# Optimization experiments

Measured on AMD Instinct MI355X. Metric: run time of the kernel, lower is better.

## Reference

```python
import jax, jax.numpy as jnp
import numpy as np

D_MODEL = 512
NUM_HEADS = 8
D_HEAD = D_MODEL // NUM_HEADS


def setup_inputs() -> dict:
    key = jax.random.key(0)
    ks = jax.random.split(key, 9)
    B, L = 4, 2048
    s = 1.0 / np.sqrt(D_MODEL)
    inp = {
        "x": jax.random.normal(ks[0], (B, L, D_MODEL), dtype=jnp.float32),
        "Wq": jax.random.uniform(ks[1], (D_MODEL, D_MODEL), jnp.float32, -s, s),
        "bq": jax.random.uniform(ks[2], (D_MODEL,), jnp.float32, -s, s),
        "Wk": jax.random.uniform(ks[3], (D_MODEL, D_MODEL), jnp.float32, -s, s),
        "bk": jax.random.uniform(ks[4], (D_MODEL,), jnp.float32, -s, s),
        "Wv": jax.random.uniform(ks[5], (D_MODEL, D_MODEL), jnp.float32, -s, s),
        "bv": jax.random.uniform(ks[6], (D_MODEL,), jnp.float32, -s, s),
        "Wo": jax.random.uniform(ks[7], (D_MODEL, D_MODEL), jnp.float32, -s, s),
        "bo": jax.random.uniform(ks[8], (D_MODEL,), jnp.float32, -s, s),
    }
    return inp


def reference(x, Wq, bq, Wk, bk, Wv, bv, Wo, bo):
    B, L, _ = x.shape
    def split_heads(t):  # [B,L,D] -> [B,H,L,d]
        return t.reshape(B, L, NUM_HEADS, D_HEAD).transpose(0, 2, 1, 3)
    Q = split_heads(x @ Wq + bq)
    K = split_heads(x @ Wk + bk)
    V = split_heads(x @ Wv + bv)
    scale = 1.0 / jnp.sqrt(jnp.asarray(D_HEAD, dtype=x.dtype))
    scores = jnp.einsum('bhqd,bhkd->bhqk', Q, K) * scale  # [B,H,L,L]
    weights = jax.nn.softmax(scores, axis=-1)
    z = jnp.einsum('bhqk,bhkd->bhqd', weights, V)  # [B,H,L,d]
    z = z.transpose(0, 2, 1, 3).reshape(B, L, D_MODEL)
    return z @ Wo + bo
```

## Files before the change

### kernel.cpp

```cpp
#include <hip/hip_runtime.h>
#include <hip/hip_bf16.h>
#include <math.h>


#define MDIM 8192
#define DMODEL 512
#define NHEAD 8
#define DHEAD 64
#define LSEQ 2048

typedef __attribute__((ext_vector_type(8))) short short8;
typedef __attribute__((ext_vector_type(4))) float floatx4;

struct alignas(16) bf16x8 { __hip_bfloat16 v[8]; };
struct alignas(8)  bf16x4 { __hip_bfloat16 v[4]; };

__device__ __forceinline__ void load_lds16(const __hip_bfloat16* g, __hip_bfloat16* l) {
    __builtin_amdgcn_global_load_lds(
        (const __attribute__((address_space(1))) void*)g,
        (__attribute__((address_space(3))) void*)l,
        16, 0, 0);
}

__device__ __forceinline__ float fast_exp2(float x) {
#if __has_builtin(__builtin_amdgcn_exp2f)
    return __builtin_amdgcn_exp2f(x);
#else
    return __expf(x * 0.69314718055994531f);
#endif
}

__global__ __launch_bounds__(256) void cast_x_kernel(
    const float* __restrict__ x, __hip_bfloat16* __restrict__ xb)
{
    size_t i = ((size_t)blockIdx.x * 256 + threadIdx.x) * 8;
    float4 a = *reinterpret_cast<const float4*>(x + i);
    float4 b = *reinterpret_cast<const float4*>(x + i + 4);
    bf16x8 o;
    o.v[0] = __float2bfloat16(a.x); o.v[1] = __float2bfloat16(a.y);
    o.v[2] = __float2bfloat16(a.z); o.v[3] = __float2bfloat16(a.w);
    o.v[4] = __float2bfloat16(b.x); o.v[5] = __float2bfloat16(b.y);
    o.v[6] = __float2bfloat16(b.z); o.v[7] = __float2bfloat16(b.w);
    *reinterpret_cast<bf16x8*>(xb + i) = o;
}

__global__ __launch_bounds__(256) void transpose_cast_w(
    const float* __restrict__ Wq, const float* __restrict__ Wk,
    const float* __restrict__ Wv, const float* __restrict__ Wo,
    __hip_bfloat16* __restrict__ Wt)
{
    __shared__ float t[32][33];
    const int z = blockIdx.z;
    const float* W = z == 0 ? Wq : (z == 1 ? Wk : (z == 2 ? Wv : Wo));
    __hip_bfloat16* dst = Wt + ((size_t)z << 18);
    int k0 = blockIdx.x * 32, n0 = blockIdx.y * 32;
    int c = threadIdx.x & 31, r = threadIdx.x >> 5;
    #pragma unroll
    for (int i = 0; i < 4; ++i)
        t[r + 8 * i][c] = W[(size_t)(k0 + r + 8 * i) * DMODEL + n0 + c];
    __syncthreads();
    #pragma unroll
    for (int i = 0; i < 4; ++i)
        dst[(size_t)(n0 + r + 8 * i) * DMODEL + k0 + c] = __float2bfloat16(t[c][r + 8 * i]);
}

__global__ __launch_bounds__(256) void gemm_qkv_mfma(
    const __hip_bfloat16* __restrict__ xb,
    const __hip_bfloat16* __restrict__ Wt,
    const float* __restrict__ bq, const float* __restrict__ bk,
    const float* __restrict__ bv,
    __hip_bfloat16* __restrict__ Q, __hip_bfloat16* __restrict__ K,
    __hip_bfloat16* __restrict__ Vt)
{
    __shared__ __hip_bfloat16 As[128 * 64];
    __shared__ __hip_bfloat16 Bs[128 * 64];

    const int tid = threadIdx.x;
    const int wid = tid >> 6, lane = tid & 63;
    const int l16 = lane & 15, quad = lane >> 4;
    const int wr = wid >> 1, wc = wid & 1;
    const int row0 = blockIdx.x * 128;
    const int which = blockIdx.y >> 2;
    const int col0 = (blockIdx.y & 3) * 128;
    const __hip_bfloat16* Wb = Wt + ((size_t)which << 18);
    const float* bias = which == 0 ? bq : (which == 1 ? bk : bv);

    const int r8 = lane >> 3, slot = lane & 7;
    const int cchunk = slot ^ (r8 & 7);

    floatx4 acc[4][4];
    #pragma unroll
    for (int i = 0; i < 4; ++i)
        #pragma unroll
        for (int j = 0; j < 4; ++j) acc[i][j] = floatx4{0.f, 0.f, 0.f, 0.f};

    for (int kt = 0; kt < DMODEL / 64; ++kt) {
        __syncthreads();
        #pragma unroll
        for (int j = 0; j < 4; ++j) {
            int seg = wid * 4 + j;
            int m = seg * 8 + r8;
            load_lds16(xb + (size_t)(row0 + m) * DMODEL + kt * 64 + cchunk * 8,
                       As + seg * 512);
            load_lds16(Wb + (size_t)(col0 + m) * DMODEL + kt * 64 + cchunk * 8,
                       Bs + seg * 512);
        }
        __syncthreads();

        #pragma unroll
        for (int ks = 0; ks < 2; ++ks) {
            const int c = ks * 4 + quad;
            short8 af[4], bf[4];
            #pragma unroll
            for (int mt = 0; mt < 4; ++mt) {
                int m = wr * 64 + mt * 16 + l16;
                af[mt] = *reinterpret_cast<const short8*>(As + m * 64 + ((c ^ (m & 7)) << 3));
            }
            #pragma unroll
            for (int nt = 0; nt < 4; ++nt) {
                int n = wc * 64 + nt * 16 + l16;
                bf[nt] = *reinterpret_cast<const short8*>(Bs + n * 64 + ((c ^ (n & 7)) << 3));
            }
            #pragma unroll
            for (int mt = 0; mt < 4; ++mt)
                #pragma unroll
                for (int nt = 0; nt < 4; ++nt)
                    acc[mt][nt] = __builtin_amdgcn_mfma_f32_16x16x32_bf16(
                        af[mt], bf[nt], acc[mt][nt], 0, 0, 0);
        }
    }

    const float QSCALE = 0.18033688011112042f;
    #pragma unroll
    for (int mt = 0; mt < 4; ++mt) {
        const int mmbase = row0 + wr * 64 + mt * 16 + quad * 4;
        const int b = mmbase >> 11;
        const int l = mmbase & 2047;
        #pragma unroll
        for (int nt = 0; nt < 4; ++nt) {
            const int nn = col0 + wc * 64 + nt * 16 + l16;
            const float bias_v = bias[nn];
            const int h = nn >> 6, dd = nn & 63;
            const int bh = b * NHEAD + h;
            if (which == 2) {
                bf16x4 pk;
                #pragma unroll
                for (int r = 0; r < 4; ++r)
                    pk.v[r] = __float2bfloat16(acc[mt][nt][r] + bias_v);
                *reinterpret_cast<bf16x4*>(Vt + ((size_t)bh * DHEAD + dd) * LSEQ + l) = pk;
            } else if (which == 0) {
                #pragma unroll
                for (int r = 0; r < 4; ++r)
                    Q[(((size_t)bh * LSEQ + l + r) << 6) + dd] =
                        __float2bfloat16((acc[mt][nt][r] + bias_v) * QSCALE);
            } else {
                #pragma unroll
                for (int r = 0; r < 4; ++r)
                    K[(((size_t)bh * LSEQ + l + r) << 6) + dd] =
                        __float2bfloat16(acc[mt][nt][r] + bias_v);
            }
        }
    }
}

__global__ __launch_bounds__(256) void gemm_out_mfma(
    const __hip_bfloat16* __restrict__ Zb,
    const __hip_bfloat16* __restrict__ WoT,
    const float* __restrict__ bo, float* __restrict__ out)
{
    __shared__ __hip_bfloat16 As[128 * 64];
    __shared__ __hip_bfloat16 Bs[128 * 64];

    const int tid = threadIdx.x;
    const int wid = tid >> 6, lane = tid & 63;
    const int l16 = lane & 15, quad = lane >> 4;
    const int wr = wid >> 1, wc = wid & 1;
    const int row0 = blockIdx.x * 128;
    const int col0 = blockIdx.y * 128;
    const int r8 = lane >> 3, slot = lane & 7;
    const int cchunk = slot ^ (r8 & 7);

    floatx4 acc[4][4];
    #pragma unroll
    for (int i = 0; i < 4; ++i)
        #pragma unroll
        for (int j = 0; j < 4; ++j) acc[i][j] = floatx4{0.f, 0.f, 0.f, 0.f};

    for (int kt = 0; kt < DMODEL / 64; ++kt) {
        __syncthreads();
        #pragma unroll
        for (int j = 0; j < 4; ++j) {
            int seg = wid * 4 + j;
            int m = seg * 8 + r8;
            load_lds16(Zb + (size_t)(row0 + m) * DMODEL + kt * 64 + cchunk * 8,
                       As + seg * 512);
            load_lds16(WoT + (size_t)(col0 + m) * DMODEL + kt * 64 + cchunk * 8,
                       Bs + seg * 512);
        }
        __syncthreads();

        #pragma unroll
        for (int ks = 0; ks < 2; ++ks) {
            const int c = ks * 4 + quad;
            short8 af[4], bf[4];
            #pragma unroll
            for (int mt = 0; mt < 4; ++mt) {
                int m = wr * 64 + mt * 16 + l16;
                af[mt] = *reinterpret_cast<const short8*>(As + m * 64 + ((c ^ (m & 7)) << 3));
            }
            #pragma unroll
            for (int nt = 0; nt < 4; ++nt) {
                int n = wc * 64 + nt * 16 + l16;
                bf[nt] = *reinterpret_cast<const short8*>(Bs + n * 64 + ((c ^ (n & 7)) << 3));
            }
            #pragma unroll
            for (int mt = 0; mt < 4; ++mt)
                #pragma unroll
                for (int nt = 0; nt < 4; ++nt)
                    acc[mt][nt] = __builtin_amdgcn_mfma_f32_16x16x32_bf16(
                        af[mt], bf[nt], acc[mt][nt], 0, 0, 0);
        }
    }

    #pragma unroll
    for (int mt = 0; mt < 4; ++mt) {
        const int mmbase = row0 + wr * 64 + mt * 16 + quad * 4;
        #pragma unroll
        for (int nt = 0; nt < 4; ++nt) {
            const int nn = col0 + wc * 64 + nt * 16 + l16;
            const float bias_v = bo[nn];
            #pragma unroll
            for (int r = 0; r < 4; ++r)
                out[(size_t)(mmbase + r) * DMODEL + nn] = acc[mt][nt][r] + bias_v;
        }
    }
}

__global__ __launch_bounds__(256) void attn_mfma(
    const __hip_bfloat16* __restrict__ Q,
    const __hip_bfloat16* __restrict__ K,
    const __hip_bfloat16* __restrict__ Vt,
    __hip_bfloat16* __restrict__ Z)
{
    __shared__ __hip_bfloat16 Qs[64 * 64];
    __shared__ __hip_bfloat16 Ks[64 * 64];
    __shared__ __hip_bfloat16 Vs[64 * 64];
    __shared__ __hip_bfloat16 Ps[4][16][72];

    const int bh = blockIdx.x >> 5;
    const int q0 = (blockIdx.x & 31) * 64;
    const int tid = threadIdx.x;
    const int wid = tid >> 6, lane = tid & 63;
    const int l16 = lane & 15, quad = lane >> 4;
    const int r8 = lane >> 3, slot = lane & 7;
    const int cchunk = slot ^ (r8 & 7);

    const __hip_bfloat16* Qg = Q + ((size_t)bh * LSEQ + q0) * DHEAD;
    const __hip_bfloat16* Kg = K + (size_t)bh * LSEQ * DHEAD;
    const __hip_bfloat16* Vg = Vt + (size_t)bh * DHEAD * LSEQ;

    #pragma unroll
    for (int j = 0; j < 2; ++j) {
        int seg = wid * 2 + j;
        int m = seg * 8 + r8;
        load_lds16(Qg + (size_t)m * DHEAD + cchunk * 8, Qs + seg * 512);
    }
    __syncthreads();

    short8 qa[2];
    {
        int m = wid * 16 + l16;
        #pragma unroll
        for (int s = 0; s < 2; ++s) {
            int c = s * 4 + quad;
            qa[s] = *reinterpret_cast<const short8*>(Qs + m * 64 + ((c ^ (m & 7)) << 3));
        }
    }

    floatx4 acc[4];
    #pragma unroll
    for (int dt = 0; dt < 4; ++dt) acc[dt] = floatx4{0.f, 0.f, 0.f, 0.f};
    float lsum = 0.f;

    for (int kt = 0; kt < LSEQ / 64; ++kt) {
        __syncthreads();
        #pragma unroll
        for (int j = 0; j < 2; ++j) {
            int seg = wid * 2 + j;
            int m = seg * 8 + r8;
            load_lds16(Kg + (size_t)(kt * 64 + m) * DHEAD + cchunk * 8, Ks + seg * 512);
            load_lds16(Vg + (size_t)m * LSEQ + kt * 64 + cchunk * 8, Vs + seg * 512);
        }
        __syncthreads();

        floatx4 sacc[4];
        #pragma unroll
        for (int nt = 0; nt < 4; ++nt) sacc[nt] = floatx4{0.f, 0.f, 0.f, 0.f};
        #pragma unroll
        for (int s = 0; s < 2; ++s) {
            #pragma unroll
            for (int nt = 0; nt < 4; ++nt) {
                int m = nt * 16 + l16;
                int c = s * 4 + quad;
                short8 kb = *reinterpret_cast<const short8*>(
                    Ks + m * 64 + ((c ^ (m & 7)) << 3));
                sacc[nt] = __builtin_amdgcn_mfma_f32_16x16x32_bf16(kb, qa[s], sacc[nt], 0, 0, 0);
            }
        }

        #pragma unroll
        for (int nt = 0; nt < 4; ++nt) {
            bf16x4 pk;
            #pragma unroll
            for (int r = 0; r < 4; ++r) {
                float p = fast_exp2(sacc[nt][r]);
                lsum += p;
                pk.v[r] = __float2bfloat16(p);
            }
            *reinterpret_cast<bf16x4*>(&Ps[wid][l16][nt * 16 + quad * 4]) = pk;
        }

        #pragma unroll
        for (int s = 0; s < 2; ++s) {
            short8 pa = *reinterpret_cast<const short8*>(&Ps[wid][l16][s * 32 + quad * 8]);
            #pragma unroll
            for (int dt = 0; dt < 4; ++dt) {
                int m = dt * 16 + l16;
                int c = s * 4 + quad;
                short8 vb = *reinterpret_cast<const short8*>(
                    Vs + m * 64 + ((c ^ (m & 7)) << 3));
                acc[dt] = __builtin_amdgcn_mfma_f32_16x16x32_bf16(pa, vb, acc[dt], 0, 0, 0);
            }
        }
    }

    lsum += __shfl_xor(lsum, 16);
    lsum += __shfl_xor(lsum, 32);
    float inv[4];
    #pragma unroll
    for (int r = 0; r < 4; ++r)
        inv[r] = 1.f / __shfl(lsum, quad * 4 + r);

    const int b = bh >> 3, h = bh & 7;
    #pragma unroll
    for (int r = 0; r < 4; ++r) {
        int qg = q0 + wid * 16 + quad * 4 + r;
        __hip_bfloat16* zr = Z + (size_t)(b * LSEQ + qg) * DMODEL + h * DHEAD;
        #pragma unroll
        for (int dt = 0; dt < 4; ++dt)
            zr[dt * 16 + l16] = __float2bfloat16(acc[dt][r] * inv[r]);
    }
}

extern "C" void kernel_launch(void* const* d_in, const int* in_sizes, int n_in,
                              void* d_out, int out_size, void* d_ws, size_t ws_size,
                              hipStream_t stream)
{
    const float* x  = (const float*)d_in[0];
    const float* Wq = (const float*)d_in[1]; const float* bq = (const float*)d_in[2];
    const float* Wk = (const float*)d_in[3]; const float* bk = (const float*)d_in[4];
    const float* Wv = (const float*)d_in[5]; const float* bv = (const float*)d_in[6];
    const float* Wo = (const float*)d_in[7]; const float* bo = (const float*)d_in[8];
    float* out = (float*)d_out;

    const size_t nqkv = (size_t)MDIM * DMODEL;
    __hip_bfloat16* xb = (__hip_bfloat16*)d_ws;
    __hip_bfloat16* Wt = xb + nqkv;
    __hip_bfloat16* Qb = Wt + ((size_t)4 << 18);
    __hip_bfloat16* Kb = Qb + nqkv;
    __hip_bfloat16* Vb = Kb + nqkv;
    __hip_bfloat16* Zb = Vb + nqkv;

    cast_x_kernel<<<dim3(MDIM * DMODEL / (256 * 8)), 256, 0, stream>>>(x, xb);
    transpose_cast_w<<<dim3(16, 16, 4), 256, 0, stream>>>(Wq, Wk, Wv, Wo, Wt);

    gemm_qkv_mfma<<<dim3(MDIM / 128, 12), 256, 0, stream>>>(
        xb, Wt, bq, bk, bv, Qb, Kb, Vb);

    attn_mfma<<<dim3(32 * (LSEQ / 64)), 256, 0, stream>>>(Qb, Kb, Vb, Zb);

    gemm_out_mfma<<<dim3(MDIM / 128, DMODEL / 128), 256, 0, stream>>>(
        Zb, Wt + ((size_t)3 << 18), bo, out);
}
```

Baseline: 178.7 us.

## Split attention keys across waves with register-resident P and LDS cross-wave reduction

The attention kernel now processes 128-key tiles, and each wave owns a 32-key slice for all 64 queries instead of 16 queries over all keys. K rows are permuted on load so the S accumulator layout feeds directly as the MFMA A operand for P·V. This removes the per-tile LDS round trip for P and halves the number of loop iterations and barriers. The price is a 4x4 output accumulator per wave, which raises register pressure, plus an epilogue that reduces partial O and row sums across waves through LDS with extra barriers.

```diff
diff --git a/kernel.cpp b/kernel.cpp
--- a/kernel.cpp
+++ b/kernel.cpp
@@ -242,10 +242,10 @@
     const __hip_bfloat16* __restrict__ Vt,
     __hip_bfloat16* __restrict__ Z)
 {
-    __shared__ __hip_bfloat16 Qs[64 * 64];
-    __shared__ __hip_bfloat16 Ks[64 * 64];
-    __shared__ __hip_bfloat16 Vs[64 * 64];
-    __shared__ __hip_bfloat16 Ps[4][16][72];
+    __shared__ __align__(16) char smem[40960];
+    __hip_bfloat16* Qs = (__hip_bfloat16*)smem;
+    __hip_bfloat16* Ks = (__hip_bfloat16*)(smem + 8192);
+    __hip_bfloat16* Vs = (__hip_bfloat16*)(smem + 24576);
 
     const int bh = blockIdx.x >> 5;
     const int q0 = (blockIdx.x & 31) * 64;
@@ -263,92 +263,126 @@
     for (int j = 0; j < 2; ++j) {
         int seg = wid * 2 + j;
         int m = seg * 8 + r8;
-        load_lds16(Qg + (size_t)m * DHEAD + cchunk * 8, Qs + seg * 512);
+        load_lds16(Qg + ((size_t)m << 6) + cchunk * 8, Qs + seg * 512);
     }
     __syncthreads();
 
-    short8 qa[2];
-    {
-        int m = wid * 16 + l16;
+    short8 qb[4][2];
+    #pragma unroll
+    for (int nt = 0; nt < 4; ++nt) {
+        int q = nt * 16 + l16;
+        #pragma unroll
+        for (int s = 0; s < 2; ++s)
+            qb[nt][s] = *reinterpret_cast<const short8*>(
+                Qs + q * 64 + (((s * 4 + quad) ^ (q & 7)) << 3));
+    }
+
+    floatx4 acc[4][4];
+    #pragma unroll
+    for (int i = 0; i < 4; ++i)
+        #pragma unroll
+        for (int j = 0; j < 4; ++j) acc[i][j] = floatx4{0.f, 0.f, 0.f, 0.f};
+    float lsum[4] = {0.f, 0.f, 0.f, 0.f};
+
+    for (int kt = 0; kt < LSEQ / 128; ++kt) {
+        __syncthreads();
+        #pragma unroll
+        for (int j = 0; j < 4; ++j) {
+            int seg = wid * 4 + j;
+            int rho = seg * 8 + r8;
+            int g = (rho & 96) | (((rho >> 2) & 3) << 3) | (((rho >> 4) & 1) << 2) | (rho & 3);
+            load_lds16(Kg + ((size_t)(kt * 128 + g) << 6) + cchunk * 8, Ks + seg * 512);
+            int d = seg * 4 + (lane >> 4);
+            int gch = (lane & 15) ^ (d & 7);
+            load_lds16(Vg + (size_t)d * LSEQ + kt * 128 + gch * 8, Vs + seg * 512);
+        }
+        __syncthreads();
+
+        floatx4 sacc[2][4];
+        #pragma unroll
+        for (int t = 0; t < 2; ++t)
+            #pragma unroll
+            for (int nt = 0; nt < 4; ++nt) sacc[t][nt] = floatx4{0.f, 0.f, 0.f, 0.f};
         #pragma unroll
         for (int s = 0; s < 2; ++s) {
-            int c = s * 4 + quad;
-            qa[s] = *reinterpret_cast<const short8*>(Qs + m * 64 + ((c ^ (m & 7)) << 3));
-        }
-    }
-
-    floatx4 acc[4];
-    #pragma unroll
-    for (int dt = 0; dt < 4; ++dt) acc[dt] = floatx4{0.f, 0.f, 0.f, 0.f};
-    float lsum = 0.f;
-
-    for (int kt = 0; kt < LSEQ / 64; ++kt) {
-        __syncthreads();
-        #pragma unroll
-        for (int j = 0; j < 2; ++j) {
-            int seg = wid * 2 + j;
-            int m = seg * 8 + r8;
-            load_lds16(Kg + (size_t)(kt * 64 + m) * DHEAD + cchunk * 8, Ks + seg * 512);
-            load_lds16(Vg + (size_t)m * LSEQ + kt * 64 + cchunk * 8, Vs + seg * 512);
-        }
-        __syncthreads();
-
-        floatx4 sacc[4];
-        #pragma unroll
-        for (int nt = 0; nt < 4; ++nt) sacc[nt] = floatx4{0.f, 0.f, 0.f, 0.f};
-        #pragma unroll
-        for (int s = 0; s < 2; ++s) {
+            const int swz = ((s * 4 + quad) ^ (l16 & 7)) << 3;
+            short8 kb0 = *reinterpret_cast<const short8*>(Ks + (wid * 32 + l16) * 64 + swz);
+            short8 kb1 = *reinterpret_cast<const short8*>(Ks + (wid * 32 + 16 + l16) * 64 + swz);
             #pragma unroll
             for (int nt = 0; nt < 4; ++nt) {
-                int m = nt * 16 + l16;
-                int c = s * 4 + quad;
-                short8 kb = *reinterpret_cast<const short8*>(
-                    Ks + m * 64 + ((c ^ (m & 7)) << 3));
-                sacc[nt] = __builtin_amdgcn_mfma_f32_16x16x32_bf16(kb, qa[s], sacc[nt], 0, 0, 0);
-            }
-        }
-
+                sacc[0][nt] = __builtin_amdgcn_mfma_f32_16x16x32_bf16(kb0, qb[nt][s], sacc[0][nt], 0, 0, 0);
+                sacc[1][nt] = __builtin_amdgcn_mfma_f32_16x16x32_bf16(kb1, qb[nt][s], sacc[1][nt], 0, 0, 0);
+            }
+        }
+
+        short8 pa[4];
         #pragma unroll
         for (int nt = 0; nt < 4; ++nt) {
-            bf16x4 pk;
-            #pragma unroll
-            for (int r = 0; r < 4; ++r) {
-                float p = fast_exp2(sacc[nt][r]);
-                lsum += p;
-                pk.v[r] = __float2bfloat16(p);
-            }
-            *reinterpret_cast<bf16x4*>(&Ps[wid][l16][nt * 16 + quad * 4]) = pk;
-        }
-
-        #pragma unroll
-        for (int s = 0; s < 2; ++s) {
-            short8 pa = *reinterpret_cast<const short8*>(&Ps[wid][l16][s * 32 + quad * 8]);
-            #pragma unroll
-            for (int dt = 0; dt < 4; ++dt) {
-                int m = dt * 16 + l16;
-                int c = s * 4 + quad;
-                short8 vb = *reinterpret_cast<const short8*>(
-                    Vs + m * 64 + ((c ^ (m & 7)) << 3));
-                acc[dt] = __builtin_amdgcn_mfma_f32_16x16x32_bf16(pa, vb, acc[dt], 0, 0, 0);
-            }
-        }
-    }
-
-    lsum += __shfl_xor(lsum, 16);
-    lsum += __shfl_xor(lsum, 32);
-    float inv[4];
-    #pragma unroll
-    for (int r = 0; r < 4; ++r)
-        inv[r] = 1.f / __shfl(lsum, quad * 4 + r);
+            union { short8 s8; __hip_bfloat16 h[8]; } u;
+            #pragma unroll
+            for (int t = 0; t < 2; ++t)
+                #pragma unroll
+                for (int r = 0; r < 4; ++r) {
+                    float p = fast_exp2(sacc[t][nt][r]);
+                    lsum[nt] += p;
+                    u.h[t * 4 + r] = __float2bfloat16(p);
+                }
+            pa[nt] = u.s8;
+        }
+
+        #pragma unroll
+        for (int dt = 0; dt < 4; ++dt) {
+            short8 vb = *reinterpret_cast<const short8*>(
+                Vs + (dt * 16 + l16) * 128 + (((wid * 4 + quad) ^ (l16 & 7)) << 3));
+            #pragma unroll
+            for (int nt = 0; nt < 4; ++nt)
+                acc[nt][dt] = __builtin_amdgcn_mfma_f32_16x16x32_bf16(pa[nt], vb, acc[nt][dt], 0, 0, 0);
+        }
+    }
+
+    __syncthreads();
+    float* Lred = (float*)smem;
+    float* Ored = (float*)(smem + 8192);
+
+    #pragma unroll
+    for (int nt = 0; nt < 4; ++nt) {
+        float v = lsum[nt];
+        v += __shfl_xor(v, 16);
+        v += __shfl_xor(v, 32);
+        lsum[nt] = v;
+    }
+    if (quad == 0) {
+        #pragma unroll
+        for (int nt = 0; nt < 4; ++nt)
+            Lred[wid * 64 + nt * 16 + l16] = lsum[nt];
+    }
 
     const int b = bh >> 3, h = bh & 7;
-    #pragma unroll
-    for (int r = 0; r < 4; ++r) {
-        int qg = q0 + wid * 16 + quad * 4 + r;
-        __hip_bfloat16* zr = Z + (size_t)(b * LSEQ + qg) * DMODEL + h * DHEAD;
-        #pragma unroll
-        for (int dt = 0; dt < 4; ++dt)
-            zr[dt * 16 + l16] = __float2bfloat16(acc[dt][r] * inv[r]);
+    const int ql = tid >> 2;
+    const int dg = tid & 3;
+    float inv = 0.f;
+
+    for (int dt = 0; dt < 4; ++dt) {
+        __syncthreads();
+        #pragma unroll
+        for (int nt = 0; nt < 4; ++nt)
+            *reinterpret_cast<floatx4*>(
+                &Ored[(wid * 16 + l16) * 68 + nt * 16 + quad * 4]) = acc[nt][dt];
+        __syncthreads();
+
+        if (dt == 0)
+            inv = 1.f / (Lred[ql] + Lred[64 + ql] + Lred[128 + ql] + Lred[192 + ql]);
+
+        bf16x4 zo;
+        #pragma unroll
+        for (int i = 0; i < 4; ++i) {
+            int d = dg * 4 + i;
+            float ssum = Ored[d * 68 + ql] + Ored[(16 + d) * 68 + ql]
+                       + Ored[(32 + d) * 68 + ql] + Ored[(48 + d) * 68 + ql];
+            zo.v[i] = __float2bfloat16(ssum * inv);
+        }
+        *reinterpret_cast<bf16x4*>(
+            Z + (size_t)(b * LSEQ + q0 + ql) * DMODEL + h * 64 + dt * 16 + dg * 4) = zo;
     }
 }
 
```

After: 177.5 us. No clear change (-0.7%).
